# Optimization experiments

Hardware: AMD Instinct MI355X
Metric: run time of the kernel (lower is better)

## Reference

```python
import jax, jax.numpy as jnp
import numpy as np

B, K, D = 16384, 20, 256
H = 4                    # attention heads
DECAY = 0.95
THRESH = 2.0             # anomaly z-score threshold
EPS = 1e-8


def setup_inputs() -> dict:
    key = jax.random.key(0)
    ks = jax.random.split(key, 10)
    s = 0.05
    return {
        "storage": jax.random.normal(ks[0], (B, K, D), jnp.float32),
        "new_message": jax.random.normal(ks[1], (B, D), jnp.float32),
        "ad_w1": jax.random.normal(ks[2], (D // 2, D), jnp.float32) * s,
        "ad_b1": jnp.zeros((D // 2,), jnp.float32),
        "ad_w2": jax.random.normal(ks[3], (1, D // 2), jnp.float32) * s,
        "ad_b2": jnp.zeros((1,), jnp.float32),
        "imp_w1": jax.random.normal(ks[4], (D, 2 * D), jnp.float32) * s,
        "imp_b1": jnp.zeros((D,), jnp.float32),
        "imp_w2": jax.random.normal(ks[5], (1, D), jnp.float32) * s,
        "imp_b2": jnp.zeros((1,), jnp.float32),
        "attn_in_w": jax.random.normal(ks[6], (3 * D, D), jnp.float32) * s,
        "attn_in_b": jnp.zeros((3 * D,), jnp.float32),
        "attn_out_w": jax.random.normal(ks[7], (D, D), jnp.float32) * s,
        "attn_out_b": jnp.zeros((D,), jnp.float32),
    }


def reference(storage, new_message, ad_w1, ad_b1, ad_w2, ad_b2,
              imp_w1, imp_b1, imp_w2, imp_b2,
              attn_in_w, attn_in_b, attn_out_w, attn_out_b):
    dt = storage.dtype
    b = storage.shape[0]
    # --- masked historical statistics over the storage slots ---
    mask = (jnp.sum(jnp.abs(storage), axis=-1) > 0).astype(dt)          # [B,K]
    denom = jnp.sum(mask, axis=1, keepdims=True) + EPS                  # [B,1]
    hmean = jnp.sum(storage * mask[..., None], axis=1) / denom          # [B,D]
    diff_sq = ((storage - hmean[:, None, :]) ** 2) * mask[..., None]
    hstd = jnp.sqrt(jnp.sum(diff_sq, axis=1) / denom)                   # [B,D]
    # --- anomaly score: statistical z-score + learned detector ---
    z = jnp.abs((new_message - hmean) / (hstd + EPS))
    stat_anom = jnp.mean((z > THRESH).astype(dt), axis=-1, keepdims=True)  # [B,1]
    h = jax.nn.relu(new_message @ ad_w1.T + ad_b1)
    learned_anom = jax.nn.sigmoid(h @ ad_w2.T + ad_b2)                  # [B,1]
    anomaly = 0.5 * stat_anom + 0.5 * learned_anom
    # --- importance weight ---
    ctx = jnp.concatenate([new_message, hmean], axis=-1)                # [B,2D]
    imp = jax.nn.softplus(jax.nn.relu(ctx @ imp_w1.T + imp_b1) @ imp_w2.T + imp_b2)
    imp = imp * (1.0 + anomaly)                                         # [B,1]
    # --- decay, roll, scatter-insert new message ---
    decay = (DECAY ** jnp.arange(K, dtype=dt))[None, :, None]           # [1,K,1]
    st = storage * decay
    st = jnp.roll(st, shift=1, axis=1)
    st = st.at[:, 0, :].set(new_message * imp)                          # [B,K,D]
    # --- multihead attention: query=new_message, key/value=storage ---
    wq, wk, wv = jnp.split(attn_in_w, 3, axis=0)
    bq, bk, bv = jnp.split(attn_in_b, 3)
    hd = D // H
    q = (new_message @ wq.T + bq).reshape(b, 1, H, hd)
    k = (st @ wk.T + bk).reshape(b, K, H, hd)
    v = (st @ wv.T + bv).reshape(b, K, H, hd)
    scores = jnp.einsum('bqhd,bkhd->bhqk', q, k) / jnp.sqrt(jnp.asarray(hd, dt))
    attn = jax.nn.softmax(scores, axis=-1)                              # [B,H,1,K]
    ctx_out = jnp.einsum('bhqk,bkhd->bqhd', attn, v).reshape(b, 1, D)
    agg = (ctx_out @ attn_out_w.T + attn_out_b)[:, 0, :]                # [B,D]
    return st, agg
```

## Files before the change

### kernel.cpp

```cpp
#include <hip/hip_runtime.h>
#include <hip/hip_bf16.h>
#include <math.h>

#define B_N 16384
#define K_N 20
#define D_N 256
#define H_N 4

typedef __attribute__((ext_vector_type(8))) short v8s;
typedef __attribute__((ext_vector_type(4))) float v4f;
typedef __hip_bfloat16 bf16;

static __device__ __forceinline__ float bf2f(bf16 x){ return __bfloat162float(x); }
static __device__ __forceinline__ bf16 f2bf(float x){ return __float2bfloat16(x); }

__global__ __launch_bounds__(256) void k_prep(
    const float* __restrict__ ad_w1, const float* __restrict__ ad_b1,
    const float* __restrict__ imp_w1, const float* __restrict__ imp_b1,
    const float* __restrict__ attn_in_w, const float* __restrict__ attn_in_b,
    const float* __restrict__ attn_out_w, const float* __restrict__ nm,
    bf16* __restrict__ attn_bf, bf16* __restrict__ impw1_bf, bf16* __restrict__ wout_bf,
    bf16* __restrict__ wcat, float* __restrict__ catb,
    float* __restrict__ g, float* __restrict__ qc,
    bf16* __restrict__ wkT, bf16* __restrict__ nm_bf)
{
    long o = (long)blockIdx.x * 256 + threadIdx.x;
    const long n_attn = 768*256, n_imp = 256*512, n_wout = 256*256, n_wcat = 640*256;
    const long n_catb = 640, n_g = 1024, n_qc = 4, n_wkT = 1024*64, n_nm = (long)B_N*256;
    if (o < n_attn){ attn_bf[o] = f2bf(attn_in_w[o]); return; } o -= n_attn;
    if (o < n_imp){ impw1_bf[o] = f2bf(imp_w1[o]); return; } o -= n_imp;
    if (o < n_wout){ wout_bf[o] = f2bf(attn_out_w[o]); return; } o -= n_wout;
    if (o < n_wcat){
        int r = (int)(o >> 8), c = (int)(o & 255); float v;
        if (r < 128)      v = ad_w1[r*256 + c];
        else if (r < 384) v = attn_in_w[(r-128)*256 + c];
        else              v = imp_w1[(r-384)*512 + c];
        wcat[o] = f2bf(v); return; } o -= n_wcat;
    if (o < n_catb){
        int r = (int)o; float v;
        if (r < 128) v = ad_b1[r]; else if (r < 384) v = attn_in_b[r-128]; else v = imp_b1[r-384];
        catb[r] = v; return; } o -= n_catb;
    if (o < n_g){
        int h = (int)(o >> 8), d = (int)(o & 255); float s = 0.f;
        for (int j = 0; j < 64; ++j) s += attn_in_w[(h*64+j)*256 + d] * attn_in_b[256 + h*64 + j];
        g[o] = s; return; } o -= n_g;
    if (o < n_qc){
        int h = (int)o; float s = 0.f;
        for (int j = 0; j < 64; ++j) s += attn_in_b[h*64+j] * attn_in_b[256 + h*64 + j];
        qc[h] = s; return; } o -= n_qc;
    if (o < n_wkT){
        int c = (int)(o >> 6), i = (int)(o & 63);
        int h = c >> 8, d = c & 255;
        wkT[o] = f2bf(attn_in_w[(256 + h*64 + i)*256 + d]); return; } o -= n_wkT;
    if (o < n_nm){ nm_bf[o] = f2bf(nm[o]); return; }
}

__global__ __launch_bounds__(256) void k_stats(const float* __restrict__ storage,
    const float* __restrict__ nm, bf16* __restrict__ hmean_bf, float* __restrict__ stat_anom)
{
    int b = blockIdx.x, t = threadIdx.x, wave = t >> 6;
    const float* S = storage + (long)b * K_N * D_N;
    float x[K_N];
    #pragma unroll
    for (int k = 0; k < K_N; ++k) x[k] = S[k*D_N + t];
    __shared__ int wnz[K_N][4];
    __shared__ int cnts[4];
    #pragma unroll
    for (int k = 0; k < K_N; ++k){
        unsigned long long bal = __ballot(x[k] != 0.0f);
        if ((t & 63) == 0) wnz[k][wave] = (bal != 0ULL) ? 1 : 0;
    }
    __syncthreads();
    float cm = 0.f, s1 = 0.f, s2 = 0.f;
    #pragma unroll
    for (int k = 0; k < K_N; ++k){
        float m = (wnz[k][0] | wnz[k][1] | wnz[k][2] | wnz[k][3]) ? 1.0f : 0.0f;
        cm += m; s1 += m * x[k]; s2 += m * x[k] * x[k];
    }
    float denom = cm + 1e-8f;
    float mu = s1 / denom;
    float var = (s2 - 2.0f*mu*s1 + mu*mu*cm) / denom;
    float sd = sqrtf(fmaxf(var, 0.0f));
    hmean_bf[(long)b*D_N + t] = f2bf(mu);
    float z = fabsf((nm[(long)b*D_N + t] - mu) / (sd + 1e-8f));
    unsigned long long bal = __ballot(z > 2.0f);
    if ((t & 63) == 0) cnts[wave] = __popcll(bal);
    __syncthreads();
    if (t == 0) stat_anom[b] = (float)(cnts[0]+cnts[1]+cnts[2]+cnts[3]) * (1.0f/256.0f);
}

__global__ __launch_bounds__(256) void k_gemm(
    const bf16* __restrict__ X, int ldx, int agshift, int agstride,
    const bf16* __restrict__ W, int ldw,
    const float* __restrict__ bias,
    const bf16* __restrict__ csrc, int ldc,
    void* __restrict__ outp, int ldo, int out_bf16,
    int relu_hi, int Kd)
{
    int wave = threadIdx.x >> 6, lane = threadIdx.x & 63;
    int l15 = lane & 15, koct = lane >> 4;
    int rblk = blockIdx.x * 64 + wave * 16;
    int cb = blockIdx.y * 64;
    long arow = rblk + l15;
    long aoff = (long)(cb >> agshift) * agstride;
    const bf16* Xp = X + arow * ldx + aoff + koct * 8;
    v4f acc[4];
    #pragma unroll
    for (int ct = 0; ct < 4; ++ct) acc[ct] = (v4f){0.f,0.f,0.f,0.f};
    for (int k0 = 0; k0 < Kd; k0 += 32){
        v8s a = *(const v8s*)(Xp + k0);
        #pragma unroll
        for (int ct = 0; ct < 4; ++ct){
            const bf16* Wp = W + (long)(cb + ct*16 + l15) * ldw + k0 + koct * 8;
            v8s bb = *(const v8s*)Wp;
            acc[ct] = __builtin_amdgcn_mfma_f32_16x16x32_bf16(a, bb, acc[ct], 0, 0, 0);
        }
    }
    int orow_base = rblk + koct * 4;
    #pragma unroll
    for (int ct = 0; ct < 4; ++ct){
        int ocol = cb + ct*16 + l15;
        float bv = bias ? bias[ocol] : 0.0f;
        #pragma unroll
        for (int r = 0; r < 4; ++r){
            long orow = orow_base + r;
            float v = acc[ct][r] + bv;
            if (csrc) v += bf2f(csrc[orow * ldc + ocol]);
            if (ocol < relu_hi) v = fmaxf(v, 0.0f);
            if (out_bf16) ((bf16*)outp)[orow * ldo + ocol] = f2bf(v);
            else          ((float*)outp)[orow * ldo + ocol] = v;
        }
    }
}

__global__ __launch_bounds__(256) void k_learned(const bf16* __restrict__ cat1,
    const float* __restrict__ ad_w2, const float* __restrict__ ad_b2, float* __restrict__ learned)
{
    int wave = threadIdx.x >> 6, lane = threadIdx.x & 63;
    long b = (long)blockIdx.x * 4 + wave;
    float p = 0.f;
    #pragma unroll
    for (int m = 0; m < 2; ++m){ int j = lane + 64*m; p += bf2f(cat1[b*640 + j]) * ad_w2[j]; }
    #pragma unroll
    for (int s = 32; s; s >>= 1) p += __shfl_xor(p, s);
    if (lane == 0) learned[b] = 1.0f / (1.0f + expf(-(p + ad_b2[0])));
}

__global__ __launch_bounds__(256) void k_imp(const bf16* __restrict__ t_bf,
    const float* __restrict__ imp_w2, const float* __restrict__ imp_b2,
    const float* __restrict__ stat_anom, const float* __restrict__ learned, float* __restrict__ imp)
{
    int wave = threadIdx.x >> 6, lane = threadIdx.x & 63;
    long b = (long)blockIdx.x * 4 + wave;
    float p = 0.f;
    #pragma unroll
    for (int m = 0; m < 4; ++m){ int j = lane + 64*m; p += bf2f(t_bf[b*256 + j]) * imp_w2[j]; }
    #pragma unroll
    for (int s = 32; s; s >>= 1) p += __shfl_xor(p, s);
    if (lane == 0){
        float x = p + imp_b2[0];
        float sp = (x > 20.0f) ? x : log1pf(expf(x));
        float an = 0.5f * stat_anom[b] + 0.5f * learned[b];
        imp[b] = sp * (1.0f + an);
    }
}

__global__ __launch_bounds__(256) void k_attn(const float* __restrict__ storage,
    const float* __restrict__ nm, const bf16* __restrict__ R_bf, const float* __restrict__ imp,
    const float* __restrict__ g, const float* __restrict__ qc,
    float* __restrict__ st_out, bf16* __restrict__ u_bf)
{
    __shared__ float stor[K_N * D_N];
    __shared__ float nm_s[D_N];
    __shared__ float R_s[H_N * D_N];
    int b = blockIdx.x, t = threadIdx.x, h = t >> 6, lane = t & 63;
    const float4* S4 = (const float4*)(storage + (long)b * K_N * D_N);
    float4* st4 = (float4*)stor;
    for (int i = t; i < K_N*D_N/4; i += 256) st4[i] = S4[i];
    nm_s[t] = nm[(long)b * D_N + t];
    for (int i = t; i < H_N*D_N; i += 256) R_s[i] = bf2f(R_bf[(long)b * H_N * D_N + i]);
    __syncthreads();
    float impv = imp[b];
    float dec[K_N-1];
    dec[0] = 1.0f;
    #pragma unroll
    for (int k = 1; k < K_N-1; ++k) dec[k] = dec[k-1] * 0.95f;
    float pq = 0.f, pr = 0.f;
    #pragma unroll
    for (int m = 0; m < 4; ++m){ int d = lane + 64*m; pq += nm_s[d]*g[h*D_N+d]; pr += nm_s[d]*R_s[h*D_N+d]; }
    #pragma unroll
    for (int s = 32; s; s >>= 1){ pq += __shfl_xor(pq, s); pr += __shfl_xor(pr, s); }
    float qb = pq + qc[h];
    float sc[K_N];
    sc[0] = (impv * pr + qb) * 0.125f;
    #pragma unroll
    for (int k = 0; k < K_N-1; ++k){
        float p = 0.f;
        #pragma unroll
        for (int m = 0; m < 4; ++m){ int d = lane + 64*m; p += stor[k*D_N+d] * R_s[h*D_N+d]; }
        #pragma unroll
        for (int s = 32; s; s >>= 1) p += __shfl_xor(p, s);
        sc[k+1] = (dec[k] * p + qb) * 0.125f;
    }
    float mx = sc[0];
    #pragma unroll
    for (int k = 1; k < K_N; ++k) mx = fmaxf(mx, sc[k]);
    float l = 0.f, w[K_N];
    #pragma unroll
    for (int k = 0; k < K_N; ++k){ w[k] = expf(sc[k]-mx); l += w[k]; }
    float inv = 1.0f / l;
    float cw[K_N-1];
    #pragma unroll
    for (int k = 0; k < K_N-1; ++k) cw[k] = w[k+1] * inv * dec[k];
    float w0 = w[0] * inv;
    #pragma unroll
    for (int m = 0; m < 4; ++m){
        int d = lane + 64*m;
        float acc = w0 * impv * nm_s[d];
        #pragma unroll
        for (int k = 0; k < K_N-1; ++k) acc += cw[k] * stor[k*D_N+d];
        u_bf[(long)b * H_N * D_N + h*D_N + d] = f2bf(acc);
    }
    float* So = st_out + (long)b * K_N * D_N;
    So[t] = impv * nm_s[t];
    #pragma unroll
    for (int k = 0; k < K_N-1; ++k) So[(k+1)*D_N + t] = stor[k*D_N + t] * dec[k];
}

extern "C" void kernel_launch(void* const* d_in, const int* in_sizes, int n_in,
                              void* d_out, int out_size, void* d_ws, size_t ws_size,
                              hipStream_t stream)
{
    (void)in_sizes; (void)n_in; (void)out_size; (void)ws_size;
    const float* storage    = (const float*)d_in[0];
    const float* nm         = (const float*)d_in[1];
    const float* ad_w1      = (const float*)d_in[2];
    const float* ad_b1      = (const float*)d_in[3];
    const float* ad_w2      = (const float*)d_in[4];
    const float* ad_b2      = (const float*)d_in[5];
    const float* imp_w1     = (const float*)d_in[6];
    const float* imp_b1     = (const float*)d_in[7];
    const float* imp_w2     = (const float*)d_in[8];
    const float* imp_b2     = (const float*)d_in[9];
    const float* attn_in_w  = (const float*)d_in[10];
    const float* attn_in_b  = (const float*)d_in[11];
    const float* attn_out_w = (const float*)d_in[12];
    const float* attn_out_b = (const float*)d_in[13];

    char* p = (char*)d_ws;
    auto alloc = [&](size_t bytes)->char*{ char* r = p; p += (bytes + 255) & ~(size_t)255; return r; };
    bf16*  attn_bf   = (bf16*) alloc((size_t)768*256*2);
    bf16*  impw1_bf  = (bf16*) alloc((size_t)256*512*2);
    bf16*  wout_bf   = (bf16*) alloc((size_t)256*256*2);
    bf16*  wcat      = (bf16*) alloc((size_t)640*256*2);
    float* catb      = (float*)alloc((size_t)640*4);
    float* g         = (float*)alloc((size_t)1024*4);
    float* qc        = (float*)alloc((size_t)4*4);
    bf16*  wkT       = (bf16*) alloc((size_t)1024*64*2);
    bf16*  nm_bf     = (bf16*) alloc((size_t)B_N*256*2);
    bf16*  hmean_bf  = (bf16*) alloc((size_t)B_N*256*2);
    float* stat_anom = (float*)alloc((size_t)B_N*4);
    bf16*  cat1      = (bf16*) alloc((size_t)B_N*640*2);
    float* learned   = (float*)alloc((size_t)B_N*4);
    bf16*  R_bf      = (bf16*) alloc((size_t)B_N*1024*2);
    bf16*  t_bf      = (bf16*) alloc((size_t)B_N*256*2);
    float* imp       = (float*)alloc((size_t)B_N*4);
    bf16*  u_bf      = (bf16*) alloc((size_t)B_N*1024*2);
    bf16*  ctx_bf    = (bf16*) alloc((size_t)B_N*256*2);

    float* st_out  = (float*)d_out;
    float* agg_out = (float*)d_out + (size_t)B_N * K_N * D_N;

    {
        long total = 768*256 + 256*512 + 256*256 + 640*256 + 640 + 1024 + 4 + 1024*64 + (long)B_N*256;
        int grid = (int)((total + 255) / 256);
        k_prep<<<grid, 256, 0, stream>>>(ad_w1, ad_b1, imp_w1, imp_b1, attn_in_w, attn_in_b,
                                         attn_out_w, nm, attn_bf, impw1_bf, wout_bf, wcat, catb,
                                         g, qc, wkT, nm_bf);
    }
    k_stats<<<B_N, 256, 0, stream>>>(storage, nm, hmean_bf, stat_anom);
    k_gemm<<<dim3(B_N/64, 640/64), 256, 0, stream>>>(nm_bf, 256, 30, 0, wcat, 256, catb,
        (const bf16*)nullptr, 0, cat1, 640, 1, 128, 256);
    k_learned<<<B_N/4, 256, 0, stream>>>(cat1, ad_w2, ad_b2, learned);
    k_gemm<<<dim3(B_N/64, 1024/64), 256, 0, stream>>>(cat1 + 128, 640, 8, 64, wkT, 64,
        (const float*)nullptr, (const bf16*)nullptr, 0, R_bf, 1024, 1, 0, 64);
    k_gemm<<<dim3(B_N/64, 256/64), 256, 0, stream>>>(hmean_bf, 256, 30, 0, impw1_bf + 256, 512,
        (const float*)nullptr, cat1 + 384, 640, t_bf, 256, 1, 256, 256);
    k_imp<<<B_N/4, 256, 0, stream>>>(t_bf, imp_w2, imp_b2, stat_anom, learned, imp);
    k_attn<<<B_N, 256, 0, stream>>>(storage, nm, R_bf, imp, g, qc, st_out, u_bf);
    k_gemm<<<dim3(B_N/64, 256/64), 256, 0, stream>>>(u_bf, 1024, 6, 256, attn_bf + 512*256, 256,
        attn_in_b + 512, (const bf16*)nullptr, 0, ctx_bf, 256, 1, 0, 256);
    k_gemm<<<dim3(B_N/64, 256/64), 256, 0, stream>>>(ctx_bf, 256, 30, 0, wout_bf, 256,
        attn_out_b, (const bf16*)nullptr, 0, agg_out, 256, 0, 0, 256);
}
```

Measured before the change: 1.024 ms.

## Vectorize k_attn loads/stores, batch shuffle reductions, write decayed storage from registers

The attention kernel now loads only the 19 storage rows that are needed and writes the decayed, rolled output directly from registers while staging the rows in shared memory. The new message, R, and g are read straight into per-lane float4 registers, and all 21 dot products are reduced together in one batched butterfly instead of serially. The context accumulation and the bf16 store now use float4/short4 vectors. The aim is to cut LDS traffic, shuffle latency chains and scalar global accesses, at the cost of higher register pressure from the 21 partial sums.

New measurement: 880.2 us. 14.0% less time.

```diff
diff --git a/kernel.cpp b/kernel.cpp
--- a/kernel.cpp
+++ b/kernel.cpp
@@ -13,6 +13,8 @@
 
 static __device__ __forceinline__ float bf2f(bf16 x){ return __bfloat162float(x); }
 static __device__ __forceinline__ bf16 f2bf(float x){ return __float2bfloat16(x); }
+static __device__ __forceinline__ float bfb2f(short s){ bf16 v; *(short*)&v = s; return __bfloat162float(v); }
+static __device__ __forceinline__ short bfbits(float x){ bf16 v = __float2bfloat16(x); return *(short*)&v; }
 
 __global__ __launch_bounds__(256) void k_prep(
     const float* __restrict__ ad_w1, const float* __restrict__ ad_b1,
@@ -170,38 +172,75 @@
     const float* __restrict__ g, const float* __restrict__ qc,
     float* __restrict__ st_out, bf16* __restrict__ u_bf)
 {
-    __shared__ float stor[K_N * D_N];
-    __shared__ float nm_s[D_N];
-    __shared__ float R_s[H_N * D_N];
+    __shared__ float4 stor4[(K_N-1) * 64];
     int b = blockIdx.x, t = threadIdx.x, h = t >> 6, lane = t & 63;
     const float4* S4 = (const float4*)(storage + (long)b * K_N * D_N);
-    float4* st4 = (float4*)stor;
-    for (int i = t; i < K_N*D_N/4; i += 256) st4[i] = S4[i];
-    nm_s[t] = nm[(long)b * D_N + t];
-    for (int i = t; i < H_N*D_N; i += 256) R_s[i] = bf2f(R_bf[(long)b * H_N * D_N + i]);
+    float4*       O4 = (float4*)(st_out + (long)b * K_N * D_N);
+
+    float impv = imp[b];
+    float4 nm4 = ((const float4*)(nm + (long)b * D_N))[lane];
+    short4 r4  = ((const short4*)(R_bf + (long)b * (H_N*D_N) + h * D_N))[lane];
+    float4 R4;
+    R4.x = bfb2f(r4.x); R4.y = bfb2f(r4.y); R4.z = bfb2f(r4.z); R4.w = bfb2f(r4.w);
+    float4 g4 = ((const float4*)(g + h * D_N))[lane];
+    float qch = qc[h];
+
+    float4 vv[5];
+    #pragma unroll
+    for (int j = 0; j < 5; ++j){
+        int i = t + j*256;
+        if (i < (K_N-1)*64) vv[j] = S4[i];
+    }
+    {
+        float dd = 1.0f;
+        int r0 = t >> 6;
+        #pragma unroll
+        for (int j = 0; j < 3; ++j) if (j < r0) dd *= 0.95f;
+        const float step = 0.81450625f;
+        #pragma unroll
+        for (int j = 0; j < 5; ++j){
+            int i = t + j*256;
+            if (i < (K_N-1)*64){
+                stor4[i] = vv[j];
+                float4 o;
+                o.x = vv[j].x * dd; o.y = vv[j].y * dd;
+                o.z = vv[j].z * dd; o.w = vv[j].w * dd;
+                O4[i + 64] = o;
+            }
+            dd *= step;
+        }
+    }
+    if (h == 0){
+        float4 o;
+        o.x = impv * nm4.x; o.y = impv * nm4.y;
+        o.z = impv * nm4.z; o.w = impv * nm4.w;
+        O4[lane] = o;
+    }
     __syncthreads();
-    float impv = imp[b];
+
+    const int NP = K_N + 1;
+    float p[NP];
+    p[0] = nm4.x*g4.x + nm4.y*g4.y + nm4.z*g4.z + nm4.w*g4.w;
+    p[1] = nm4.x*R4.x + nm4.y*R4.y + nm4.z*R4.z + nm4.w*R4.w;
+    #pragma unroll
+    for (int k = 0; k < K_N-1; ++k){
+        float4 x = stor4[k*64 + lane];
+        p[2+k] = x.x*R4.x + x.y*R4.y + x.z*R4.z + x.w*R4.w;
+    }
+    #pragma unroll
+    for (int s = 32; s; s >>= 1){
+        #pragma unroll
+        for (int j = 0; j < NP; ++j) p[j] += __shfl_xor(p[j], s);
+    }
     float dec[K_N-1];
     dec[0] = 1.0f;
     #pragma unroll
     for (int k = 1; k < K_N-1; ++k) dec[k] = dec[k-1] * 0.95f;
-    float pq = 0.f, pr = 0.f;
-    #pragma unroll
-    for (int m = 0; m < 4; ++m){ int d = lane + 64*m; pq += nm_s[d]*g[h*D_N+d]; pr += nm_s[d]*R_s[h*D_N+d]; }
-    #pragma unroll
-    for (int s = 32; s; s >>= 1){ pq += __shfl_xor(pq, s); pr += __shfl_xor(pr, s); }
-    float qb = pq + qc[h];
+    float qb = p[0] + qch;
     float sc[K_N];
-    sc[0] = (impv * pr + qb) * 0.125f;
-    #pragma unroll
-    for (int k = 0; k < K_N-1; ++k){
-        float p = 0.f;
-        #pragma unroll
-        for (int m = 0; m < 4; ++m){ int d = lane + 64*m; p += stor[k*D_N+d] * R_s[h*D_N+d]; }
-        #pragma unroll
-        for (int s = 32; s; s >>= 1) p += __shfl_xor(p, s);
-        sc[k+1] = (dec[k] * p + qb) * 0.125f;
-    }
+    sc[0] = (impv * p[1] + qb) * 0.125f;
+    #pragma unroll
+    for (int k = 0; k < K_N-1; ++k) sc[k+1] = (dec[k] * p[2+k] + qb) * 0.125f;
     float mx = sc[0];
     #pragma unroll
     for (int k = 1; k < K_N; ++k) mx = fmaxf(mx, sc[k]);
@@ -209,22 +248,21 @@
     #pragma unroll
     for (int k = 0; k < K_N; ++k){ w[k] = expf(sc[k]-mx); l += w[k]; }
     float inv = 1.0f / l;
+    float w0 = w[0] * inv * impv;
     float cw[K_N-1];
     #pragma unroll
     for (int k = 0; k < K_N-1; ++k) cw[k] = w[k+1] * inv * dec[k];
-    float w0 = w[0] * inv;
-    #pragma unroll
-    for (int m = 0; m < 4; ++m){
-        int d = lane + 64*m;
-        float acc = w0 * impv * nm_s[d];
-        #pragma unroll
-        for (int k = 0; k < K_N-1; ++k) acc += cw[k] * stor[k*D_N+d];
-        u_bf[(long)b * H_N * D_N + h*D_N + d] = f2bf(acc);
-    }
-    float* So = st_out + (long)b * K_N * D_N;
-    So[t] = impv * nm_s[t];
-    #pragma unroll
-    for (int k = 0; k < K_N-1; ++k) So[(k+1)*D_N + t] = stor[k*D_N + t] * dec[k];
+
+    float4 acc;
+    acc.x = w0 * nm4.x; acc.y = w0 * nm4.y; acc.z = w0 * nm4.z; acc.w = w0 * nm4.w;
+    #pragma unroll
+    for (int k = 0; k < K_N-1; ++k){
+        float4 x = stor4[k*64 + lane];
+        acc.x += cw[k]*x.x; acc.y += cw[k]*x.y; acc.z += cw[k]*x.z; acc.w += cw[k]*x.w;
+    }
+    short4 us;
+    us.x = bfbits(acc.x); us.y = bfbits(acc.y); us.z = bfbits(acc.z); us.w = bfbits(acc.w);
+    ((short4*)(u_bf + (long)b * (H_N*D_N) + h * D_N))[lane] = us;
 }
 
 extern "C" void kernel_launch(void* const* d_in, const int* in_sizes, int n_in,
```
